# Performance work log

Hardware: AMD Instinct MI355X
Metric: run time of the kernel (lower is better)

## Reference

```python
import jax, jax.numpy as jnp
import numpy as np

BN_EPS = 1e-5
EPS = 1e-6


def _conv(x, w, pad, dil):
    # NCHW dilated conv, stride 1, no bias (matches nn.Conv2d(bias=False))
    return jax.lax.conv_general_dilated(
        x, w, window_strides=(1, 1), padding=[(pad, pad), (pad, pad)],
        rhs_dilation=(dil, dil), dimension_numbers=('NCHW', 'OIHW', 'NCHW'))


def _bn_relu(x, s, b, m, v):
    # eval-mode batchnorm (running stats) + relu
    inv = (s / jnp.sqrt(v + BN_EPS))[None, :, None, None]
    return jax.nn.relu((x - m[None, :, None, None]) * inv + b[None, :, None, None])


def _l2n(x):
    # l2_norm over channel dim (dim=-2 of [B,C,N]); no eps, as in source
    return x / jnp.linalg.norm(x, axis=1, keepdims=True)


def _forward(x, w1, w2, w3, w4, bn_scale, bn_bias, bn_mean, bn_var,
             wq, bq, wk, bk, wv, bv, gamma):
    B, C, H, W = x.shape
    N = H * W
    # HASP: four dilated-conv branches (dilations 1,6,12,18), concat to 128 ch
    specs = [(w1, 0, 1), (w2, 6, 6), (w3, 12, 12), (w4, 18, 18)]
    branches = [_bn_relu(_conv(x, w, p, d), bn_scale[i], bn_bias[i],
                         bn_mean[i], bn_var[i])
                for i, (w, p, d) in enumerate(specs)]
    x_q = jnp.concatenate(branches, axis=1)  # [B,128,H,W]
    # 1x1 convs as channel GEMMs
    Q = (jnp.einsum('oi,bihw->bohw', wq[:, :, 0, 0], x_q)
         + bq[None, :, None, None]).reshape(B, -1, N)  # [B,16,N]
    K = (jnp.einsum('oi,bihw->bohw', wk[:, :, 0, 0], x)
         + bk[None, :, None, None]).reshape(B, -1, N)  # [B,16,N]
    V = (jnp.einsum('oi,bihw->bohw', wv[:, :, 0, 0], x)
         + bv[None, :, None, None]).reshape(B, -1, N)  # [B,128,N]
    Qn = _l2n(Q).transpose(0, 2, 1)  # [B,N,16]
    Kn = _l2n(K)                     # [B,16,N]
    tailor = 1.0 / (N + jnp.einsum('bnm,bm->bn', Qn, Kn.sum(-1) + EPS))  # [B,N]
    vsum = V.sum(-1)[:, :, None]                      # [B,128,1]
    mat = jnp.einsum('bmn,bcn->bmc', Kn, V)           # [B,16,128]
    msum = vsum + jnp.einsum('bnm,bmc->bcn', Qn, mat)  # [B,128,N]
    out = (msum * tailor[:, None, :]).reshape(B, C, H, W)
    return gamma * out


def setup_inputs() -> dict:
    key = jax.random.key(0)
    ks = jax.random.split(key, 12)
    B, C, H, W = 8, 128, 128, 128
    M = 16  # in_places // scale
    d = {
        'x': jax.random.normal(ks[0], (B, C, H, W), jnp.float32),
        'w1': jax.random.normal(ks[1], (32, 128, 1, 1), jnp.float32) * 0.05,
        'w2': jax.random.normal(ks[2], (32, 128, 3, 3), jnp.float32) * 0.05,
        'w3': jax.random.normal(ks[3], (32, 128, 3, 3), jnp.float32) * 0.05,
        'w4': jax.random.normal(ks[4], (32, 128, 3, 3), jnp.float32) * 0.05,
        'bn_scale': jnp.ones((4, 32), jnp.float32),
        'bn_bias': jnp.zeros((4, 32), jnp.float32),
        'bn_mean': jnp.zeros((4, 32), jnp.float32),
        'bn_var': jnp.ones((4, 32), jnp.float32),
        'wq': jax.random.normal(ks[5], (M, 128, 1, 1), jnp.float32) * 0.05,
        'bq': jax.random.normal(ks[6], (M,), jnp.float32) * 0.05,
        'wk': jax.random.normal(ks[7], (M, 128, 1, 1), jnp.float32) * 0.05,
        'bk': jax.random.normal(ks[8], (M,), jnp.float32) * 0.05,
        'wv': jax.random.normal(ks[9], (C, 128, 1, 1), jnp.float32) * 0.05,
        'bv': jax.random.normal(ks[10], (C,), jnp.float32) * 0.05,
        'gamma': jax.random.uniform(ks[11], (1,), jnp.float32),
    }
    return d


def reference(x, w1, w2, w3, w4, bn_scale, bn_bias, bn_mean, bn_var,
              wq, bq, wk, bk, wv, bv, gamma):
    return _forward(x, w1, w2, w3, w4, bn_scale, bn_bias, bn_mean, bn_var,
                    wq, bq, wk, bk, wv, bv, gamma)
```

## Files before the change

kernel.cpp:

```cpp
#include <hip/hip_runtime.h>
#include <hip/hip_bf16.h>
#include <math.h>

#define NPIX   16384
#define BATCH  8
#define BN_EPS 1e-5f
#define EPS_V  1e-6f

typedef __attribute__((ext_vector_type(8))) short bf16x8;
typedef __attribute__((ext_vector_type(4))) float f32x4;
typedef const __attribute__((address_space(1))) unsigned int* gas_ptr;
typedef __attribute__((address_space(3))) unsigned int* las_ptr;

#define OFF_K     ((size_t)0)
#define OFF_PART2 ((size_t)8192)
#define OFF_W1F   ((size_t)2097152)
#define OFF_WKT   ((size_t)2101248)
#define OFF_WVT   ((size_t)2103296)
#define OFF_BF    ((size_t)2119680)
#define OFF_PART  ((size_t)2119808)
#define OFF_STATS ((size_t)3242112)
#define BASE_END  ((size_t)3259648)
#define OFF_WBT   BASE_END
#define OFF_XT    ((size_t)3314976)
#define OFF_WVB   ((size_t)11703584)
#define OFF_ZROW  ((size_t)11711776)
#define NEW_END   ((size_t)11713824)
#define OFF_W24T  BASE_END

__device__ inline unsigned short f2bf(float f) {
  union { float f; unsigned int u; } v; v.f = f;
  unsigned int r = (v.u + 0x7FFFu + ((v.u >> 16) & 1u)) >> 16;
  return (unsigned short)r;
}

__global__ void prep_common_kernel(const float* __restrict__ w1,
                                   const float* __restrict__ bns, const float* __restrict__ bnb,
                                   const float* __restrict__ bnm, const float* __restrict__ bnv,
                                   const float* __restrict__ wk, const float* __restrict__ wv,
                                   float* __restrict__ w1f, float* __restrict__ wkt,
                                   float* __restrict__ wvt, float* __restrict__ bf) {
  int tid = blockIdx.x * blockDim.x + threadIdx.x;
  int nt  = gridDim.x * blockDim.x;
  for (int i = tid; i < 128; i += nt) {
    float inv = bns[i] * rsqrtf(bnv[i] + BN_EPS);
    bf[i] = bnb[i] - bnm[i] * inv;
  }
  for (int i = tid; i < 4096; i += nt) {
    int c = i >> 5, o = i & 31;
    float inv = bns[o] * rsqrtf(bnv[o] + BN_EPS);
    w1f[i] = w1[o * 128 + c] * inv;
  }
  for (int i = tid; i < 2048; i += nt) {
    int c = i >> 4, m = i & 15;
    wkt[i] = wk[m * 128 + c];
  }
  for (int i = tid; i < 16384; i += nt) {
    int c = i >> 7, o = i & 127;
    wvt[i] = wv[o * 128 + c];
  }
}

__global__ void prep_convb_kernel(const float* __restrict__ w1,
                                  const float* __restrict__ w2, const float* __restrict__ w3,
                                  const float* __restrict__ w4,
                                  const float* __restrict__ bns, const float* __restrict__ bnv,
                                  const float* __restrict__ wk, const float* __restrict__ wv,
                                  unsigned short* __restrict__ wbtr,
                                  unsigned short* __restrict__ wvbr,
                                  unsigned short* __restrict__ wxbr,
                                  unsigned short* __restrict__ zrow) {
  int tid = blockIdx.x * blockDim.x + threadIdx.x;
  int nt  = gridDim.x * blockDim.x;
  for (int i = tid; i < 4096; i += nt) zrow[i] = 0;
  for (int i = tid; i < 16384; i += nt) {
    int e = i & 7, lane = (i >> 3) & 63, f = (i >> 9) & 7, q = i >> 12;
    int oc = f * 16 + (lane & 15);
    int c  = q * 32 + (lane >> 4) * 8 + e;
    wvbr[i] = f2bf(wv[oc * 128 + c]);
  }
  for (int i = tid; i < 6144; i += nt) {
    int e = i & 7, lane = (i >> 3) & 63, ct = i >> 9;
    int tile = ct % 3, q = ct / 3;
    int c = q * 32 + (lane >> 4) * 8 + e;
    float val;
    if (tile < 2) {
      int oc = tile * 16 + (lane & 15);
      val = w1[oc * 128 + c] * (bns[oc] * rsqrtf(bnv[oc] + BN_EPS));
    } else {
      val = wk[(lane & 15) * 128 + c];
    }
    wxbr[i] = f2bf(val);
  }
  for (int i = tid; i < 110592; i += nt) {
    int br = i / 36864;
    int r  = i - br * 36864;
    int tap  = r >> 12;
    int r2   = r & 4095;
    int q    = r2 >> 10;
    int r3   = r2 & 1023;
    int pair = r3 >> 9;
    int r4   = r3 & 511;
    int lane = r4 >> 3, e = r4 & 7;
    int oc = pair * 16 + (lane & 15);
    int c  = q * 32 + (lane >> 4) * 8 + e;
    const float* w = (br == 0) ? w2 : ((br == 1) ? w3 : w4);
    int bo = (br + 1) * 32 + oc;
    float inv = bns[bo] * rsqrtf(bnv[bo] + BN_EPS);
    wbtr[i] = f2bf(w[(oc * 128 + c) * 9 + tap] * inv);
  }
}

__global__ void prep_convf_kernel(const float* __restrict__ w2, const float* __restrict__ w3,
                                  const float* __restrict__ w4,
                                  const float* __restrict__ bns, const float* __restrict__ bnv,
                                  float* __restrict__ w24t) {
  int tid = blockIdx.x * blockDim.x + threadIdx.x;
  int nt  = gridDim.x * blockDim.x;
  for (int i = tid; i < 110592; i += nt) {
    int br  = i / 36864;
    int rem = i - br * 36864;
    int c   = rem / 288;
    int k   = (rem % 288) >> 5;
    int o   = rem & 31;
    const float* w = (br == 0) ? w2 : ((br == 1) ? w3 : w4);
    int bo = (br + 1) * 32 + o;
    float inv = bns[bo] * rsqrtf(bnv[bo] + BN_EPS);
    w24t[i] = w[(o * 128 + c) * 9 + k] * inv;
  }
}

__global__ __launch_bounds__(256) void a0_kernel(const float* __restrict__ x,
                                                 unsigned short* __restrict__ xt) {
  __shared__ unsigned short Ts[64][132];
  int t   = threadIdx.x;
  int b   = blockIdx.y;
  int px0 = blockIdx.x * 64;
  const float* xb = x + (size_t)b * 128 * NPIX;
  int p = t & 63, cq = t >> 6;
#pragma unroll 8
  for (int i = 0; i < 32; ++i) {
    int c = cq * 32 + i;
    Ts[p][c] = f2bf(xb[(size_t)c * NPIX + px0 + p]);
  }
  __syncthreads();
  int pw = t >> 2, cg = t & 3;
  unsigned short* dst = xt + ((size_t)(b * 4 + cg) * 16384 + px0 + pw) * 32;
  int sw = (pw >> 1) & 3;
#pragma unroll
  for (int k = 0; k < 8; ++k) {
    uint2 v = *(const uint2*)(&Ts[pw][cg * 32 + k * 4]);
    int cgs = (k >> 1) ^ sw;
    *(uint2*)(dst + cgs * 8 + (k & 1) * 4) = v;
  }
}

__global__ __launch_bounds__(256) void a1_kernel(const float* __restrict__ x,
                                                 const float* __restrict__ w1f,
                                                 const float* __restrict__ wkt,
                                                 const float* __restrict__ bfp,
                                                 const float* __restrict__ bk,
                                                 float* __restrict__ out,
                                                 float* __restrict__ Kbuf) {
  __shared__ float lw1[128 * 32];
  __shared__ float lwk[128 * 16];
  __shared__ float lbf[32];
  int t = threadIdx.x;
  for (int i = t; i < 4096; i += 256) lw1[i] = w1f[i];
  for (int i = t; i < 2048; i += 256) lwk[i] = wkt[i];
  if (t < 32) lbf[t] = bfp[t];
  __syncthreads();

  int b  = blockIdx.y;
  int px = blockIdx.x * 256 + t;
  const float* xb = x + (size_t)b * 128 * NPIX;

  float acc[48];
#pragma unroll
  for (int i = 0; i < 48; ++i) acc[i] = 0.f;

  for (int c = 0; c < 128; ++c) {
    float xv = xb[(size_t)c * NPIX + px];
    const float4* w1p = (const float4*)(lw1 + c * 32);
#pragma unroll
    for (int j = 0; j < 8; ++j) {
      float4 w = w1p[j];
      acc[j*4+0] = fmaf(w.x, xv, acc[j*4+0]);
      acc[j*4+1] = fmaf(w.y, xv, acc[j*4+1]);
      acc[j*4+2] = fmaf(w.z, xv, acc[j*4+2]);
      acc[j*4+3] = fmaf(w.w, xv, acc[j*4+3]);
    }
    const float4* wkp = (const float4*)(lwk + c * 16);
#pragma unroll
    for (int j = 0; j < 4; ++j) {
      float4 w = wkp[j];
      acc[32+j*4+0] = fmaf(w.x, xv, acc[32+j*4+0]);
      acc[32+j*4+1] = fmaf(w.y, xv, acc[32+j*4+1]);
      acc[32+j*4+2] = fmaf(w.z, xv, acc[32+j*4+2]);
      acc[32+j*4+3] = fmaf(w.w, xv, acc[32+j*4+3]);
    }
  }
#pragma unroll
  for (int o = 0; o < 32; ++o)
    out[((size_t)(b * 128 + o)) * NPIX + px] = fmaxf(acc[o] + lbf[o], 0.f);
#pragma unroll
  for (int m = 0; m < 16; ++m)
    Kbuf[((size_t)(b * 16 + m)) * NPIX + px] = acc[32 + m] + bk[m];
}

__global__ __launch_bounds__(256) void a2m_kernel(const unsigned short* __restrict__ xt,
                                                  const unsigned short* __restrict__ zrow,
                                                  const unsigned short* __restrict__ wbtr,
                                                  const float* __restrict__ bfp,
                                                  float* __restrict__ out) {
  __shared__ unsigned short sx[3 * 8192 + 8];
  int t    = threadIdx.x;
  int wave = t >> 6, lane = t & 63;
  int l15  = lane & 15, cg = lane >> 4;
  int idx  = blockIdx.x;
  int b    = idx & 7;
  int rest = idx >> 3;
  int h2   = rest & 63;
  int br   = rest >> 6;
  int d    = 6 * (br + 1);
  int h0   = h2 * 2;
  int j    = wave >> 1;
  int whalf = wave & 1;
  int p0   = whalf * 64;

  if (t == 0) *(uint4*)(sx + 24576) = make_uint4(0u, 0u, 0u, 0u);

  const unsigned short* wb    = wbtr + (size_t)br * 36864;
  const unsigned short* slabs = xt + (size_t)b * 4 * 524288;

  f32x4 acc[2][4];
#pragma unroll
  for (int i = 0; i < 2; ++i)
#pragma unroll
    for (int n = 0; n < 4; ++n) acc[i][n] = (f32x4){0.f, 0.f, 0.f, 0.f};

  int pxb[3], xorv[3];
#pragma unroll
  for (int kw = 0; kw < 3; ++kw) {
    pxb[kw]  = p0 + l15 + (kw - 1) * d;
    xorv[kw] = (cg ^ ((pxb[kw] >> 1) & 3)) << 4;
  }

  auto STAGE = [&](int s) {
    int q = s / 3, kh = s % 3;
    int srow = h0 + j + (kh - 1) * d;
    const unsigned short* rowsrc =
        ((unsigned)srow < 128u) ? (slabs + (size_t)q * 524288 + (size_t)srow * 4096)
                                : zrow;
    const unsigned short* gsrc = rowsrc + whalf * 2048 + lane * 8;
    unsigned short* lbase = sx + (s % 3) * 8192 + j * 4096 + whalf * 2048;
#pragma unroll
    for (int k = 0; k < 4; ++k)
      __builtin_amdgcn_global_load_lds((gas_ptr)(const void*)(gsrc + k * 512),
                                       (las_ptr)(void*)(lbase + k * 512), 16, 0, 0);
  };

  auto COMPUTE = [&](int s) {
    int q = s / 3, kh = s % 3;
    int bb = (s % 3) * 16384 + j * 8192;
    bf16x8 a[3][2];
#pragma unroll
    for (int kw = 0; kw < 3; ++kw) {
      int tap = kh * 3 + kw;
      const unsigned short* wt = wb + ((((size_t)tap * 4 + q) * 2) << 9);
      a[kw][0] = *(const bf16x8*)(wt + lane * 8);
      a[kw][1] = *(const bf16x8*)(wt + 512 + lane * 8);
    }
#pragma unroll
    for (int kw = 0; kw < 3; ++kw) {
      int base = bb + pxb[kw] * 64 + xorv[kw];
#pragma unroll
      for (int nf = 0; nf < 4; ++nf) {
        int px   = pxb[kw] + nf * 16;
        int addr = ((unsigned)px < 128u) ? (base + nf * 1024) : 49152;
        bf16x8 bv = *(const bf16x8*)((const char*)sx + addr);
        acc[0][nf] = __builtin_amdgcn_mfma_f32_16x16x32_bf16(a[kw][0], bv, acc[0][nf], 0, 0, 0);
        acc[1][nf] = __builtin_amdgcn_mfma_f32_16x16x32_bf16(a[kw][1], bv, acc[1][nf], 0, 0, 0);
      }
    }
  };

  STAGE(0);
  STAGE(1);
  __syncthreads();
  for (int s = 0; s < 12; ++s) {
    COMPUTE(s);
    if (s < 10) STAGE(s + 2);
    if (s < 11) {
      if (s < 10) asm volatile("s_waitcnt vmcnt(4)" ::: "memory");
      else        asm volatile("s_waitcnt vmcnt(0)" ::: "memory");
      __builtin_amdgcn_s_barrier();
      __builtin_amdgcn_sched_barrier(0);
    }
  }

  int ocb = (br + 1) * 32;
  int pxw = (h0 + j) * 128 + p0;
#pragma unroll
  for (int mf = 0; mf < 2; ++mf) {
#pragma unroll
    for (int r = 0; r < 4; ++r) {
      int oc = mf * 16 + cg * 4 + r;
      float bias = bfp[ocb + oc];
      float* op = out + ((size_t)(b * 128 + ocb + oc)) * NPIX + pxw + l15;
#pragma unroll
      for (int nf = 0; nf < 4; ++nf)
        op[nf * 16] = fmaxf(acc[mf][nf][r] + bias, 0.f);
    }
  }
}

__global__ __launch_bounds__(256) void a2f_kernel(const float* __restrict__ x,
                                                  const float* __restrict__ w24t,
                                                  const float* __restrict__ bfp,
                                                  float* __restrict__ out) {
  int t  = threadIdx.x;
  int og = t & 3;
  int pg = (t >> 2) & 15;
  int r  = t >> 6;
  int br = blockIdx.z;
  int b  = blockIdx.y;
  int h  = blockIdx.x * 4 + r;
  int d  = 6 * (br + 1);

  const float* wt = w24t + (size_t)br * 36864;
  const float* bf = bfp + (br + 1) * 32;
  const float* xb = x + (size_t)b * 128 * NPIX;
  int w0 = pg << 3;

  float acc[8][8];
#pragma unroll
  for (int p = 0; p < 8; ++p)
#pragma unroll
    for (int o = 0; o < 8; ++o) acc[p][o] = 0.f;

  for (int c = 0; c < 128; ++c) {
    const float* xc = xb + (size_t)c * NPIX;
    const float* wc = wt + c * 288;
#pragma unroll
    for (int kh = 0; kh < 3; ++kh) {
      int row = h + (kh - 1) * d;
      if ((unsigned)row >= 128u) continue;
      const float* xr = xc + row * 128;
#pragma unroll
      for (int kw = 0; kw < 3; ++kw) {
        int wb = w0 + (kw - 1) * d;
        float xv[8];
        if (wb >= 0 && wb <= 120) {
          const float2* p2 = (const float2*)(xr + wb);
#pragma unroll
          for (int jj = 0; jj < 4; ++jj) {
            float2 v = p2[jj];
            xv[2*jj] = v.x; xv[2*jj+1] = v.y;
          }
        } else {
#pragma unroll
          for (int jj = 0; jj < 8; ++jj) {
            int ww = wb + jj;
            xv[jj] = ((unsigned)ww < 128u) ? xr[ww] : 0.f;
          }
        }
        const float4* wp = (const float4*)(wc + (kh * 3 + kw) * 32 + og * 8);
        float4 wa = wp[0], wbv = wp[1];
        float wr[8] = {wa.x, wa.y, wa.z, wa.w, wbv.x, wbv.y, wbv.z, wbv.w};
#pragma unroll
        for (int p = 0; p < 8; ++p)
#pragma unroll
          for (int o = 0; o < 8; ++o)
            acc[p][o] = fmaf(xv[p], wr[o], acc[p][o]);
      }
    }
  }

  int chbase = (br + 1) * 32 + og * 8;
  int n = h * 128 + w0;
#pragma unroll
  for (int o = 0; o < 8; ++o) {
    float bias = bf[og * 8 + o];
    float* op = out + ((size_t)(b * 128 + chbase + o)) * NPIX + n;
    float4 v0 = make_float4(fmaxf(acc[0][o] + bias, 0.f), fmaxf(acc[1][o] + bias, 0.f),
                            fmaxf(acc[2][o] + bias, 0.f), fmaxf(acc[3][o] + bias, 0.f));
    float4 v1 = make_float4(fmaxf(acc[4][o] + bias, 0.f), fmaxf(acc[5][o] + bias, 0.f),
                            fmaxf(acc[6][o] + bias, 0.f), fmaxf(acc[7][o] + bias, 0.f));
    ((float4*)op)[0] = v0;
    ((float4*)op)[1] = v1;
  }
}

__global__ __launch_bounds__(256) void cm_kernel(const unsigned short* __restrict__ xt,
                                                 const unsigned short* __restrict__ wvbr,
                                                 const unsigned short* __restrict__ wxbr,
                                                 const float* __restrict__ bv,
                                                 const float* __restrict__ bfp,
                                                 const float* __restrict__ bk,
                                                 float* __restrict__ out,
                                                 float* __restrict__ part1,
                                                 float* __restrict__ part2) {
  __shared__ __align__(16) unsigned short Vl[128 * 136];
  __shared__ __align__(16) unsigned short knl[16 * 136];
  int t    = threadIdx.x;
  int idx  = blockIdx.x;
  int b    = idx & 7;
  int blk  = idx >> 3;
  int wave = t >> 6, lane = t & 63;
  int l15  = lane & 15, cg = lane >> 4;
  int ocb  = wave * 32;
  int pbase = blk << 7;
  int cgsw = (cg ^ ((l15 >> 1) & 3)) << 3;

  float bvr[2][4];
#pragma unroll
  for (int mf = 0; mf < 2; ++mf)
#pragma unroll
    for (int r = 0; r < 4; ++r) bvr[mf][r] = bv[ocb + mf * 16 + cg * 4 + r];

  float xb4[4];
#pragma unroll
  for (int r = 0; r < 4; ++r) xb4[r] = 0.f;
  if (wave == 0) {
#pragma unroll
    for (int r = 0; r < 4; ++r) xb4[r] = bfp[cg * 4 + r];
  } else if (wave == 1) {
#pragma unroll
    for (int r = 0; r < 4; ++r) xb4[r] = bfp[16 + cg * 4 + r];
  } else if (wave == 2) {
#pragma unroll
    for (int r = 0; r < 4; ++r) xb4[r] = bk[cg * 4 + r];
  }
  int xwave = (wave < 3) ? wave : 0;

  float kr[4] = {0.f, 0.f, 0.f, 0.f};
  float sv[2][4];
#pragma unroll
  for (int mf = 0; mf < 2; ++mf)
#pragma unroll
    for (int r = 0; r < 4; ++r) sv[mf][r] = 0.f;
  f32x4 am[2];
  am[0] = (f32x4){0.f,0.f,0.f,0.f};
  am[1] = (f32x4){0.f,0.f,0.f,0.f};

#pragma unroll
  for (int hf = 0; hf < 2; ++hf) {
    f32x4 vacc[2][4];
    f32x4 xacc[4];
#pragma unroll
    for (int i = 0; i < 2; ++i)
#pragma unroll
      for (int n = 0; n < 4; ++n) vacc[i][n] = (f32x4){0.f,0.f,0.f,0.f};
#pragma unroll
    for (int n = 0; n < 4; ++n) xacc[n] = (f32x4){0.f,0.f,0.f,0.f};

#pragma unroll
    for (int cc = 0; cc < 4; ++cc) {
      const unsigned short* xq = xt + ((size_t)(b * 4 + cc) * 16384 + pbase) * 32;
      bf16x8 a0 = *(const bf16x8*)(wvbr + ((cc * 8 + wave * 2 + 0) << 9) + lane * 8);
      bf16x8 a1 = *(const bf16x8*)(wvbr + ((cc * 8 + wave * 2 + 1) << 9) + lane * 8);
      bf16x8 ax = *(const bf16x8*)(wxbr + ((cc * 3 + xwave) << 9) + lane * 8);
#pragma unroll
      for (int nf = 0; nf < 4; ++nf) {
        int nfg = hf * 4 + nf;
        bf16x8 bx = *(const bf16x8*)(xq + (size_t)(nfg * 16 + l15) * 32 + cgsw);
        vacc[0][nf] = __builtin_amdgcn_mfma_f32_16x16x32_bf16(a0, bx, vacc[0][nf], 0, 0, 0);
        vacc[1][nf] = __builtin_amdgcn_mfma_f32_16x16x32_bf16(a1, bx, vacc[1][nf], 0, 0, 0);
        if (wave < 3)
          xacc[nf] = __builtin_amdgcn_mfma_f32_16x16x32_bf16(ax, bx, xacc[nf], 0, 0, 0);
      }
    }

#pragma unroll
    for (int mf = 0; mf < 2; ++mf) {
#pragma unroll
      for (int r = 0; r < 4; ++r) {
        float s = 0.f;
#pragma unroll
        for (int nf = 0; nf < 4; ++nf) s += vacc[mf][nf][r];
        sv[mf][r] += s;
        int c = ocb + mf * 16 + cg * 4 + r;
#pragma unroll
        for (int nf = 0; nf < 4; ++nf)
          Vl[c * 136 + (hf * 4 + nf) * 16 + l15] = f2bf(vacc[mf][nf][r] + bvr[mf][r]);
      }
    }

    if (wave < 2) {
#pragma unroll
      for (int r = 0; r < 4; ++r) {
        int oc = wave * 16 + cg * 4 + r;
        float* op = out + ((size_t)(b * 128 + oc)) * NPIX + pbase + l15;
#pragma unroll
        for (int nf = 0; nf < 4; ++nf)
          op[(hf * 4 + nf) * 16] = fmaxf(xacc[nf][r] + xb4[r], 0.f);
      }
    } else if (wave == 2) {
#pragma unroll
      for (int nf = 0; nf < 4; ++nf) {
        int nfg = hf * 4 + nf;
        float kq[4]; float s2 = 0.f;
#pragma unroll
        for (int r = 0; r < 4; ++r) {
          kq[r] = xacc[nf][r] + xb4[r];
          s2 = fmaf(kq[r], kq[r], s2);
        }
        s2 += __shfl_xor(s2, 16);
        s2 += __shfl_xor(s2, 32);
        float inv = rsqrtf(s2);
#pragma unroll
        for (int r = 0; r < 4; ++r) {
          float kn = kq[r] * inv;
          knl[(cg * 4 + r) * 136 + nfg * 16 + l15] = f2bf(kn);
          kr[r] += kn;
        }
      }
    }
  }
  __syncthreads();

#pragma unroll
  for (int ks = 0; ks < 4; ++ks) {
    bf16x8 af = *(const bf16x8*)(knl + l15 * 136 + ks * 32 + cg * 8);
    bf16x8 b0 = *(const bf16x8*)(Vl + (size_t)(ocb + l15) * 136 + ks * 32 + cg * 8);
    bf16x8 b1 = *(const bf16x8*)(Vl + (size_t)(ocb + 16 + l15) * 136 + ks * 32 + cg * 8);
    am[0] = __builtin_amdgcn_mfma_f32_16x16x32_bf16(af, b0, am[0], 0, 0, 0);
    am[1] = __builtin_amdgcn_mfma_f32_16x16x32_bf16(af, b1, am[1], 0, 0, 0);
  }

  float* pp = (blk < 64) ? (part1 + ((size_t)b * 64 + blk) * 2192)
                         : (part2 + ((size_t)b * 64 + (blk - 64)) * 2192);
#pragma unroll
  for (int nf2 = 0; nf2 < 2; ++nf2)
#pragma unroll
    for (int r = 0; r < 4; ++r)
      pp[(cg * 4 + r) * 128 + ocb + nf2 * 16 + l15] = am[nf2][r];
#pragma unroll
  for (int off = 1; off < 16; off <<= 1) {
#pragma unroll
    for (int mf = 0; mf < 2; ++mf)
#pragma unroll
      for (int r = 0; r < 4; ++r)
        sv[mf][r] += __shfl_xor(sv[mf][r], off);
  }
  if (l15 == 0) {
#pragma unroll
    for (int mf = 0; mf < 2; ++mf)
#pragma unroll
      for (int r = 0; r < 4; ++r) {
        int c = ocb + mf * 16 + cg * 4 + r;
        pp[2048 + c] = sv[mf][r] + 128.f * bv[c];
      }
  }
  if (wave == 2) {
#pragma unroll
    for (int off = 1; off < 16; off <<= 1) {
#pragma unroll
      for (int r = 0; r < 4; ++r)
        kr[r] += __shfl_xor(kr[r], off);
    }
    if (l15 == 0) {
#pragma unroll
      for (int r = 0; r < 4; ++r)
        pp[2048 + 128 + cg * 4 + r] = kr[r];
    }
  }
}

__global__ __launch_bounds__(256) void cf_kernel(const float* __restrict__ x,
                                                 const float* __restrict__ bv,
                                                 const float* __restrict__ Kbuf,
                                                 const float* __restrict__ wvt,
                                                 float* __restrict__ part) {
  __shared__ float Vl[128 * 129];
  __shared__ float knl[16 * 132];
  int t   = threadIdx.x;
  int b   = blockIdx.y;
  int blk = blockIdx.x;
  const float* Kb = Kbuf + (size_t)b * 16 * NPIX;
  const float* xb = x + (size_t)b * 128 * NPIX;

  int m_own = t & 15;
  int c0    = (t >> 4) << 3;
  int pxg   = t & 15;

  float bvr[8];
#pragma unroll
  for (int jj = 0; jj < 8; ++jj) bvr[jj] = bv[c0 + jj];

  float macc[8] = {0,0,0,0,0,0,0,0};
  float vs[8]   = {0,0,0,0,0,0,0,0};
  float ksum[16];
#pragma unroll
  for (int m = 0; m < 16; ++m) ksum[m] = 0.f;

  for (int tile = blk; tile < 128; tile += 64) {
    __syncthreads();
    int pbase = tile << 7;

    if (t < 128) {
      float kv[16]; float ss = 0.f;
#pragma unroll
      for (int m = 0; m < 16; ++m) {
        kv[m] = Kb[(size_t)m * NPIX + pbase + t];
        ss = fmaf(kv[m], kv[m], ss);
      }
      float inv = rsqrtf(ss);
#pragma unroll
      for (int m = 0; m < 16; ++m) {
        float kn = kv[m] * inv;
        knl[m * 132 + t] = kn;
        ksum[m] += kn;
      }
    }

    float v[8][8];
#pragma unroll
    for (int i = 0; i < 8; ++i)
#pragma unroll
      for (int jj = 0; jj < 8; ++jj) v[i][jj] = 0.f;
    int px0 = pbase + (pxg << 3);
    for (int k = 0; k < 128; ++k) {
      const float4* xp = (const float4*)(xb + (size_t)k * NPIX + px0);
      float4 xa = xp[0], xc4 = xp[1];
      const float4* wp = (const float4*)(wvt + k * 128 + c0);
      float4 wa = wp[0], wc4 = wp[1];
      float xv[8] = {xa.x, xa.y, xa.z, xa.w, xc4.x, xc4.y, xc4.z, xc4.w};
      float wr[8] = {wa.x, wa.y, wa.z, wa.w, wc4.x, wc4.y, wc4.z, wc4.w};
#pragma unroll
      for (int i = 0; i < 8; ++i)
#pragma unroll
        for (int jj = 0; jj < 8; ++jj)
          v[i][jj] = fmaf(wr[i], xv[jj], v[i][jj]);
    }
#pragma unroll
    for (int i = 0; i < 8; ++i)
#pragma unroll
      for (int jj = 0; jj < 8; ++jj)
        Vl[(c0 + i) * 129 + (pxg << 3) + jj] = v[i][jj] + bvr[i];
    __syncthreads();

    for (int px = 0; px < 128; ++px) {
      float knv = knl[m_own * 132 + px];
      float vv[8];
#pragma unroll
      for (int jj = 0; jj < 8; ++jj) vv[jj] = Vl[(c0 + jj) * 129 + px];
#pragma unroll
      for (int jj = 0; jj < 8; ++jj) macc[jj] = fmaf(knv, vv[jj], macc[jj]);
      if (m_own == 0) {
#pragma unroll
        for (int jj = 0; jj < 8; ++jj) vs[jj] += vv[jj];
      }
    }
  }

  int blkid = b * 64 + blk;
  float* pp = part + (size_t)blkid * 2192;
#pragma unroll
  for (int jj = 0; jj < 8; ++jj) pp[m_own * 128 + c0 + jj] = macc[jj];
  if (m_own == 0) {
#pragma unroll
    for (int jj = 0; jj < 8; ++jj) pp[2048 + c0 + jj] = vs[jj];
  }
  __syncthreads();
  if (t < 128) {
#pragma unroll
    for (int m = 0; m < 16; ++m) knl[m * 132 + t] = ksum[m];
  }
  __syncthreads();
  if (t < 16) {
    float s = 0.f;
    for (int i = 0; i < 128; ++i) s += knl[t * 132 + i];
    pp[2048 + 128 + t] = s;
  }
}

__global__ void reduce_kernel(const float* __restrict__ part, float* __restrict__ stats) {
  int b = blockIdx.y, t = threadIdx.x;
  int e = blockIdx.x * 256 + t;
  if (e >= 2192) return;
  const float* pp = part + (size_t)b * 64 * 2192;
  float s = 0.f;
  for (int g = 0; g < 64; ++g) s += pp[(size_t)g * 2192 + e];
  stats[(size_t)b * 2192 + e] = s;
}

__global__ void reduce2_kernel(const float* __restrict__ part1,
                               const float* __restrict__ part2,
                               float* __restrict__ stats) {
  int b = blockIdx.y, t = threadIdx.x;
  int e = blockIdx.x * 256 + t;
  if (e >= 2192) return;
  const float* p1 = part1 + (size_t)b * 64 * 2192;
  const float* p2 = part2 + (size_t)b * 64 * 2192;
  float s = 0.f;
  for (int g = 0; g < 64; ++g) s += p1[(size_t)g * 2192 + e];
  for (int g = 0; g < 64; ++g) s += p2[(size_t)g * 2192 + e];
  stats[(size_t)b * 2192 + e] = s;
}

__global__ __launch_bounds__(256) void df_kernel(const float* __restrict__ stats,
                                                 const float* __restrict__ wq,
                                                 const float* __restrict__ bq,
                                                 const float* __restrict__ gamma,
                                                 float* __restrict__ out) {
  __shared__ float matl[128 * 16];
  __shared__ float wql[128 * 16];
  __shared__ float vsl[128];
  __shared__ float ksl[16];
  int t = threadIdx.x;
  int b = blockIdx.y;
  const float* st = stats + (size_t)b * 2192;
  for (int i = t; i < 2048; i += 256) {
    int m = i >> 7, c = i & 127;
    matl[c * 16 + m] = st[i];
    wql[c * 16 + m]  = wq[m * 128 + c];
  }
  if (t < 128) vsl[t] = st[2048 + t];
  if (t < 16)  ksl[t] = st[2048 + 128 + t] + EPS_V;
  __syncthreads();

  int px = blockIdx.x * 256 + t;
  float* ob = out + (size_t)b * 128 * NPIX;

  float q[16];
#pragma unroll
  for (int m = 0; m < 16; ++m) q[m] = bq[m];
  for (int c = 0; c < 128; ++c) {
    float xv = ob[(size_t)c * NPIX + px];
    const float4* wp = (const float4*)(wql + c * 16);
#pragma unroll
    for (int jj = 0; jj < 4; ++jj) {
      float4 w = wp[jj];
      q[jj*4+0] = fmaf(w.x, xv, q[jj*4+0]);
      q[jj*4+1] = fmaf(w.y, xv, q[jj*4+1]);
      q[jj*4+2] = fmaf(w.z, xv, q[jj*4+2]);
      q[jj*4+3] = fmaf(w.w, xv, q[jj*4+3]);
    }
  }
  float ss = 0.f;
#pragma unroll
  for (int m = 0; m < 16; ++m) ss = fmaf(q[m], q[m], ss);
  float inv = rsqrtf(ss);
#pragma unroll
  for (int m = 0; m < 16; ++m) q[m] *= inv;
  float den = (float)NPIX;
#pragma unroll
  for (int m = 0; m < 16; ++m) den = fmaf(q[m], ksl[m], den);
  float tl = gamma[0] / den;

  for (int c = 0; c < 128; ++c) {
    float s = vsl[c];
    const float4* mp = (const float4*)(matl + c * 16);
#pragma unroll
    for (int jj = 0; jj < 4; ++jj) {
      float4 w = mp[jj];
      s = fmaf(w.x, q[jj*4+0], s);
      s = fmaf(w.y, q[jj*4+1], s);
      s = fmaf(w.z, q[jj*4+2], s);
      s = fmaf(w.w, q[jj*4+3], s);
    }
    ob[(size_t)c * NPIX + px] = tl * s;
  }
}

extern "C" void kernel_launch(void* const* d_in, const int* in_sizes, int n_in,
                              void* d_out, int out_size, void* d_ws, size_t ws_size,
                              hipStream_t stream) {
  (void)in_sizes; (void)n_in; (void)out_size;
  const float* x   = (const float*)d_in[0];
  const float* w1  = (const float*)d_in[1];
  const float* w2  = (const float*)d_in[2];
  const float* w3  = (const float*)d_in[3];
  const float* w4  = (const float*)d_in[4];
  const float* bns = (const float*)d_in[5];
  const float* bnb = (const float*)d_in[6];
  const float* bnm = (const float*)d_in[7];
  const float* bnv = (const float*)d_in[8];
  const float* wq  = (const float*)d_in[9];
  const float* bq  = (const float*)d_in[10];
  const float* wk  = (const float*)d_in[11];
  const float* bk  = (const float*)d_in[12];
  const float* wv  = (const float*)d_in[13];
  const float* bv  = (const float*)d_in[14];
  const float* gm  = (const float*)d_in[15];
  float* ws  = (float*)d_ws;
  float* out = (float*)d_out;

  float* Kbuf = ws + OFF_K;
  float* w1f  = ws + OFF_W1F;
  float* wkt  = ws + OFF_WKT;
  float* wvt  = ws + OFF_WVT;
  float* bfp  = ws + OFF_BF;
  float* part = ws + OFF_PART;
  float* stat = ws + OFF_STATS;

  prep_common_kernel<<<64, 256, 0, stream>>>(w1, bns, bnb, bnm, bnv, wk, wv,
                                             w1f, wkt, wvt, bfp);

  bool use_mfma = ws_size >= NEW_END * sizeof(float);
  if (use_mfma) {
    unsigned short* wbtr = (unsigned short*)(ws + OFF_WBT);
    unsigned short* xt   = (unsigned short*)(ws + OFF_XT);
    unsigned short* wvbr = (unsigned short*)(ws + OFF_WVB);
    unsigned short* zrow = (unsigned short*)(ws + OFF_ZROW);
    unsigned short* wxbr = (unsigned short*)(ws + OFF_K);
    float* part2 = ws + OFF_PART2;
    prep_convb_kernel<<<64, 256, 0, stream>>>(w1, w2, w3, w4, bns, bnv, wk, wv,
                                              wbtr, wvbr, wxbr, zrow);
    a0_kernel<<<dim3(256, 8), 256, 0, stream>>>(x, xt);
    a2m_kernel<<<dim3(1536), 256, 0, stream>>>(xt, zrow, wbtr, bfp, out);
    cm_kernel<<<dim3(1024), 256, 0, stream>>>(xt, wvbr, wxbr, bv, bfp, bk, out, part, part2);
    reduce2_kernel<<<dim3(9, 8), 256, 0, stream>>>(part, part2, stat);
    df_kernel<<<dim3(64, 8), 256, 0, stream>>>(stat, wq, bq, gm, out);
  } else {
    float* w24t = ws + OFF_W24T;
    prep_convf_kernel<<<64, 256, 0, stream>>>(w2, w3, w4, bns, bnv, w24t);
    a1_kernel<<<dim3(64, 8), 256, 0, stream>>>(x, w1f, wkt, bfp, bk, out, Kbuf);
    a2f_kernel<<<dim3(32, 8, 3), 256, 0, stream>>>(x, w24t, bfp, out);
    cf_kernel<<<dim3(64, 8), 256, 0, stream>>>(x, bv, Kbuf, wvt, part);
    reduce_kernel<<<dim3(9, 8), 256, 0, stream>>>(part, stat);
    df_kernel<<<dim3(64, 8), 256, 0, stream>>>(stat, wq, bq, gm, out);
  }
}
```

Measured before the change: 138.5 us.

## Shrink a2m LDS to double buffer and fold bias prep into convb prep

The dilated-conv MFMA kernel drops from a triple-buffered to a double-buffered LDS staging scheme. Out-of-range pixels are now handled by masking the loaded value to zero rather than reading a dedicated zero slot, which lowers LDS per block and may allow more blocks per CU. The prefetch now runs only one stage ahead with a full vmcnt(0) wait each iteration, which reduces how much load latency is hidden. The fused BN bias computation moves into prep_convb, removing the separate prep_common launch on the MFMA path.

```diff
diff --git a/kernel.cpp b/kernel.cpp
--- a/kernel.cpp
+++ b/kernel.cpp
@@ -64,14 +64,20 @@
 __global__ void prep_convb_kernel(const float* __restrict__ w1,
                                   const float* __restrict__ w2, const float* __restrict__ w3,
                                   const float* __restrict__ w4,
-                                  const float* __restrict__ bns, const float* __restrict__ bnv,
+                                  const float* __restrict__ bns, const float* __restrict__ bnb,
+                                  const float* __restrict__ bnm, const float* __restrict__ bnv,
                                   const float* __restrict__ wk, const float* __restrict__ wv,
                                   unsigned short* __restrict__ wbtr,
                                   unsigned short* __restrict__ wvbr,
                                   unsigned short* __restrict__ wxbr,
-                                  unsigned short* __restrict__ zrow) {
+                                  unsigned short* __restrict__ zrow,
+                                  float* __restrict__ bf) {
   int tid = blockIdx.x * blockDim.x + threadIdx.x;
   int nt  = gridDim.x * blockDim.x;
+  for (int i = tid; i < 128; i += nt) {
+    float inv = bns[i] * rsqrtf(bnv[i] + BN_EPS);
+    bf[i] = bnb[i] - bnm[i] * inv;
+  }
   for (int i = tid; i < 4096; i += nt) zrow[i] = 0;
   for (int i = tid; i < 16384; i += nt) {
     int e = i & 7, lane = (i >> 3) & 63, f = (i >> 9) & 7, q = i >> 12;
@@ -213,7 +219,7 @@
                                                   const unsigned short* __restrict__ wbtr,
                                                   const float* __restrict__ bfp,
                                                   float* __restrict__ out) {
-  __shared__ unsigned short sx[3 * 8192 + 8];
+  __shared__ unsigned short sx[2 * 8192];
   int t    = threadIdx.x;
   int wave = t >> 6, lane = t & 63;
   int l15  = lane & 15, cg = lane >> 4;
@@ -228,8 +234,6 @@
   int whalf = wave & 1;
   int p0   = whalf * 64;
 
-  if (t == 0) *(uint4*)(sx + 24576) = make_uint4(0u, 0u, 0u, 0u);
-
   const unsigned short* wb    = wbtr + (size_t)br * 36864;
   const unsigned short* slabs = xt + (size_t)b * 4 * 524288;
 
@@ -253,7 +257,7 @@
         ((unsigned)srow < 128u) ? (slabs + (size_t)q * 524288 + (size_t)srow * 4096)
                                 : zrow;
     const unsigned short* gsrc = rowsrc + whalf * 2048 + lane * 8;
-    unsigned short* lbase = sx + (s % 3) * 8192 + j * 4096 + whalf * 2048;
+    unsigned short* lbase = sx + (s & 1) * 8192 + j * 4096 + whalf * 2048;
 #pragma unroll
     for (int k = 0; k < 4; ++k)
       __builtin_amdgcn_global_load_lds((gas_ptr)(const void*)(gsrc + k * 512),
@@ -262,7 +266,7 @@
 
   auto COMPUTE = [&](int s) {
     int q = s / 3, kh = s % 3;
-    int bb = (s % 3) * 16384 + j * 8192;
+    int bb = (s & 1) * 16384 + j * 8192;
     bf16x8 a[3][2];
 #pragma unroll
     for (int kw = 0; kw < 3; ++kw) {
@@ -276,9 +280,14 @@
       int base = bb + pxb[kw] * 64 + xorv[kw];
 #pragma unroll
       for (int nf = 0; nf < 4; ++nf) {
-        int px   = pxb[kw] + nf * 16;
-        int addr = ((unsigned)px < 128u) ? (base + nf * 1024) : 49152;
-        bf16x8 bv = *(const bf16x8*)((const char*)sx + addr);
+        int px      = pxb[kw] + nf * 16;
+        bool ok     = ((unsigned)px < 128u);
+        int addr    = ok ? (base + nf * 1024) : bb;
+        unsigned m  = ok ? 0xFFFFFFFFu : 0u;
+        uint4 u = *(const uint4*)((const char*)sx + addr);
+        u.x &= m; u.y &= m; u.z &= m; u.w &= m;
+        bf16x8 bv;
+        __builtin_memcpy(&bv, &u, 16);
         acc[0][nf] = __builtin_amdgcn_mfma_f32_16x16x32_bf16(a[kw][0], bv, acc[0][nf], 0, 0, 0);
         acc[1][nf] = __builtin_amdgcn_mfma_f32_16x16x32_bf16(a[kw][1], bv, acc[1][nf], 0, 0, 0);
       }
@@ -286,14 +295,14 @@
   };
 
   STAGE(0);
-  STAGE(1);
-  __syncthreads();
+  asm volatile("s_waitcnt vmcnt(0)" ::: "memory");
+  __builtin_amdgcn_s_barrier();
+  __builtin_amdgcn_sched_barrier(0);
   for (int s = 0; s < 12; ++s) {
+    if (s < 11) STAGE(s + 1);
     COMPUTE(s);
-    if (s < 10) STAGE(s + 2);
     if (s < 11) {
-      if (s < 10) asm volatile("s_waitcnt vmcnt(4)" ::: "memory");
-      else        asm volatile("s_waitcnt vmcnt(0)" ::: "memory");
+      asm volatile("s_waitcnt vmcnt(0)" ::: "memory");
       __builtin_amdgcn_s_barrier();
       __builtin_amdgcn_sched_barrier(0);
     }
@@ -796,9 +805,6 @@
   float* part = ws + OFF_PART;
   float* stat = ws + OFF_STATS;
 
-  prep_common_kernel<<<64, 256, 0, stream>>>(w1, bns, bnb, bnm, bnv, wk, wv,
-                                             w1f, wkt, wvt, bfp);
-
   bool use_mfma = ws_size >= NEW_END * sizeof(float);
   if (use_mfma) {
     unsigned short* wbtr = (unsigned short*)(ws + OFF_WBT);
@@ -807,8 +813,8 @@
     unsigned short* zrow = (unsigned short*)(ws + OFF_ZROW);
     unsigned short* wxbr = (unsigned short*)(ws + OFF_K);
     float* part2 = ws + OFF_PART2;
-    prep_convb_kernel<<<64, 256, 0, stream>>>(w1, w2, w3, w4, bns, bnv, wk, wv,
-                                              wbtr, wvbr, wxbr, zrow);
+    prep_convb_kernel<<<64, 256, 0, stream>>>(w1, w2, w3, w4, bns, bnb, bnm, bnv, wk, wv,
+                                              wbtr, wvbr, wxbr, zrow, bfp);
     a0_kernel<<<dim3(256, 8), 256, 0, stream>>>(x, xt);
     a2m_kernel<<<dim3(1536), 256, 0, stream>>>(xt, zrow, wbtr, bfp, out);
     cm_kernel<<<dim3(1024), 256, 0, stream>>>(xt, wvbr, wxbr, bv, bfp, bk, out, part, part2);
@@ -816,6 +822,8 @@
     df_kernel<<<dim3(64, 8), 256, 0, stream>>>(stat, wq, bq, gm, out);
   } else {
     float* w24t = ws + OFF_W24T;
+    prep_common_kernel<<<64, 256, 0, stream>>>(w1, bns, bnb, bnm, bnv, wk, wv,
+                                               w1f, wkt, wvt, bfp);
     prep_convf_kernel<<<64, 256, 0, stream>>>(w2, w3, w4, bns, bnv, w24t);
     a1_kernel<<<dim3(64, 8), 256, 0, stream>>>(x, w1f, wkt, bfp, bk, out, Kbuf);
     a2f_kernel<<<dim3(32, 8, 3), 256, 0, stream>>>(x, w24t, bfp, out);
```

Measured after the change: 137.9 us. About the same (-0.4%).
